# Optimization experiments

Hardware: AMD Instinct MI355X
Metric: run time of the kernel (lower is better)

Reference implementation:

```python
import jax, jax.numpy as jnp
import numpy as np

DECAY = 0.99


def setup_inputs() -> dict:
    key = jax.random.key(0)
    k1, k2, k3 = jax.random.split(key, 3)
    B, D, H, W = 16, 128, 32, 32
    K = 8192
    z_e = jax.random.normal(k1, (B, D, H, W), dtype=jnp.float32)
    codebook = jax.random.normal(k2, (K, D), dtype=jnp.float32)
    ema_count = jnp.ones((K,), dtype=jnp.float32)
    ema_weight = codebook  # buffer initialized as codebook.clone()
    return {"z_e": z_e, "codebook": codebook, "ema_count": ema_count, "ema_weight": ema_weight}


def reference(z_e, codebook, ema_count, ema_weight):
    B, D, H, W = z_e.shape
    K = codebook.shape[0]
    # (B,D,H,W) -> (N,D)
    z_flat = z_e.transpose(0, 2, 3, 1).reshape(-1, D)
    # squared L2 distances: ||z||^2 - 2 z.C^T + ||C||^2  -> (N,K)
    dist = (
        jnp.sum(z_flat * z_flat, axis=1, keepdims=True)
        - 2.0 * (z_flat @ codebook.T)
        + jnp.sum(codebook * codebook, axis=1)[None, :]
    )
    indices = jnp.argmin(dist, axis=1)  # (N,)
    z_q = codebook[indices].reshape(B, H, W, D).transpose(0, 3, 1, 2)
    # EMA codebook update (training path, no grad)
    counts = jax.ops.segment_sum(jnp.ones_like(indices, dtype=jnp.float32), indices, num_segments=K)
    dw = jax.ops.segment_sum(z_flat, indices, num_segments=K)  # (K,D)
    new_count = ema_count * DECAY + (1.0 - DECAY) * counts
    new_weight = ema_weight * DECAY + (1.0 - DECAY) * dw
    new_codebook = new_weight / jnp.maximum(new_count, 1.0)[:, None]
    # straight-through estimator
    z_q_st = z_e + jax.lax.stop_gradient(z_q - z_e)
    return (z_q_st, indices.reshape(B, H, W), new_codebook, new_count, new_weight)
```

## Files before the change

### kernel.cpp

```cpp
#include <hip/hip_runtime.h>

#define D 128
#define HW 1024
#define NROWS 16384
#define K 8192

#define OUT0 0
#define OUT1 2097152
#define OUT2 2113536
#define OUT3 3162112
#define OUT4 3170304

typedef __attribute__((ext_vector_type(8))) _Float16 half8;
typedef __attribute__((ext_vector_type(16))) float f32x16;
typedef unsigned short u16;
typedef unsigned long long u64;

__device__ __forceinline__ void gld16(const u16* gsrc, u16* ldst) {
    __builtin_amdgcn_global_load_lds(
        (const __attribute__((address_space(1))) unsigned int*)gsrc,
        (__attribute__((address_space(3))) unsigned int*)ldst,
        16, 0, 0);
}

__global__ __launch_bounds__(256) void k_cnorm(const float* __restrict__ cb,
                                               float* __restrict__ cnorm) {
    int lane = threadIdx.x & 63;
    int k = blockIdx.x * 4 + (threadIdx.x >> 6);
    float2 v = *(const float2*)(cb + (size_t)k * D + lane * 2);
    float s = v.x * v.x + v.y * v.y;
#pragma unroll
    for (int off = 32; off > 0; off >>= 1) s += __shfl_down(s, off);
    if (lane == 0) cnorm[k] = s;
}

__global__ __launch_bounds__(256) void k_prep_cb(const float* __restrict__ cb,
                                                 u16* __restrict__ Bh, u16* __restrict__ Bl) {
    int gid = blockIdx.x * 256 + threadIdx.x;
    int k  = gid & (K - 1);
    int kk = gid >> 13;
    const float* src = cb + (size_t)k * D + kk * 8;
    half8 h, l;
#pragma unroll
    for (int j = 0; j < 8; ++j) {
        float v = src[j];
        _Float16 hv = (_Float16)v;
        _Float16 lv = (_Float16)(v - (float)hv);
        h[j] = hv;
        l[j] = lv;
    }
    size_t off = ((((size_t)(k >> 8) * 8 + (kk >> 1)) * 2 + (kk & 1)) * 256 + (k & 255)) * 8;
    *(half8*)(Bh + off) = h;
    *(half8*)(Bl + off) = l;
}

__global__ __launch_bounds__(256) void k_prep_z(const float* __restrict__ z_e,
                                                u16* __restrict__ Ah, u16* __restrict__ Al) {
    int gid = blockIdx.x * 256 + threadIdx.x;
    int n  = gid & (NROWS - 1);
    int kk = gid >> 14;
    int b = n >> 10, hw = n & 1023;
    const float* src = z_e + ((size_t)b * D + kk * 8) * HW + hw;
    half8 h, l;
#pragma unroll
    for (int j = 0; j < 8; ++j) {
        float v = src[(size_t)j * HW];
        _Float16 hv = (_Float16)v;
        _Float16 lv = (_Float16)(v - (float)hv);
        h[j] = hv;
        l[j] = lv;
    }
    int rg = n >> 7, band = (n >> 5) & 3, row = n & 31;
    size_t off = (((((size_t)rg * 4 + band) * 8 + (kk >> 1)) * 2 + (kk & 1)) * 32 + row) * 8;
    *(half8*)(Ah + off) = h;
    *(half8*)(Al + off) = l;
}

__global__ __launch_bounds__(256, 1) void k_argmin_mfma(
        const u16* __restrict__ Ahg, const u16* __restrict__ Alg,
        const u16* __restrict__ Bhg, const u16* __restrict__ Blg,
        const float* __restrict__ cnorm, u64* __restrict__ packed) {
    __shared__ u16 lds[65536];
    u16* AhL = lds;
    u16* AlL = lds + 16384;
    u16* BL  = lds + 32768;

    const int tid = threadIdx.x;
    const int ln  = tid & 63;
    const int l31 = ln & 31;
    const int lh  = ln >> 5;
    const int wy  = (tid >> 6) & 1;
    const int wx  = tid >> 7;

    const int rg = blockIdx.x >> 2;
    const int k0 = (blockIdx.x & 3) * 2048;

    {
        const u16* s0 = Ahg + (size_t)rg * 16384;
        const u16* s1 = Alg + (size_t)rg * 16384;
#pragma unroll
        for (int r = 0; r < 8; ++r) {
            gld16(s0 + (r * 256 + tid) * 8, AhL + (r * 256 + tid) * 8);
            gld16(s1 + (r * 256 + tid) * 8, AlL + (r * 256 + tid) * 8);
        }
    }
    asm volatile("s_waitcnt vmcnt(0)" ::: "memory");
    __syncthreads();

    float minv[2][16];
    int   mini[2][16];
#pragma unroll
    for (int rt = 0; rt < 2; ++rt)
#pragma unroll
        for (int r = 0; r < 16; ++r) { minv[rt][r] = INFINITY; mini[rt][r] = 0; }

#pragma unroll 1
    for (int cg = 0; cg < 8; ++cg) {
        const int colbase = k0 + cg * 256;
        const size_t gB = (size_t)((k0 >> 8) + cg) * 32768;
        f32x16 acc[2][4] = {};

#pragma unroll
        for (int r = 0; r < 16; ++r)
            gld16(Blg + gB + (r * 256 + tid) * 8, BL + (r * 256 + tid) * 8);
        asm volatile("s_waitcnt vmcnt(0)" ::: "memory");
        __syncthreads();
#pragma unroll
        for (int ks = 0; ks < 8; ++ks) {
            half8 b[4], a[2];
#pragma unroll
            for (int c = 0; c < 4; ++c)
                b[c] = *(const half8*)(BL + (((ks * 2 + lh) * 256) + wx * 128 + c * 32 + l31) * 8);
#pragma unroll
            for (int rt = 0; rt < 2; ++rt)
                a[rt] = *(const half8*)(AhL + ((((wy * 2 + rt) * 8 + ks) * 2 + lh) * 32 + l31) * 8);
#pragma unroll
            for (int rt = 0; rt < 2; ++rt)
#pragma unroll
                for (int c = 0; c < 4; ++c)
                    acc[rt][c] = __builtin_amdgcn_mfma_f32_32x32x16_f16(a[rt], b[c], acc[rt][c], 0, 0, 0);
        }
        __syncthreads();

#pragma unroll
        for (int r = 0; r < 16; ++r)
            gld16(Bhg + gB + (r * 256 + tid) * 8, BL + (r * 256 + tid) * 8);

        float cn[4];
#pragma unroll
        for (int c = 0; c < 4; ++c) cn[c] = cnorm[colbase + wx * 128 + c * 32 + l31];

        asm volatile("s_waitcnt vmcnt(0)" ::: "memory");
        __syncthreads();
#pragma unroll
        for (int ks = 0; ks < 8; ++ks) {
            half8 b[4], a[2], al[2];
#pragma unroll
            for (int c = 0; c < 4; ++c)
                b[c] = *(const half8*)(BL + (((ks * 2 + lh) * 256) + wx * 128 + c * 32 + l31) * 8);
#pragma unroll
            for (int rt = 0; rt < 2; ++rt) {
                a[rt]  = *(const half8*)(AhL + ((((wy * 2 + rt) * 8 + ks) * 2 + lh) * 32 + l31) * 8);
                al[rt] = *(const half8*)(AlL + ((((wy * 2 + rt) * 8 + ks) * 2 + lh) * 32 + l31) * 8);
            }
#pragma unroll
            for (int rt = 0; rt < 2; ++rt)
#pragma unroll
                for (int c = 0; c < 4; ++c)
                    acc[rt][c] = __builtin_amdgcn_mfma_f32_32x32x16_f16(a[rt], b[c], acc[rt][c], 0, 0, 0);
#pragma unroll
            for (int rt = 0; rt < 2; ++rt)
#pragma unroll
                for (int c = 0; c < 4; ++c)
                    acc[rt][c] = __builtin_amdgcn_mfma_f32_32x32x16_f16(al[rt], b[c], acc[rt][c], 0, 0, 0);
        }

#pragma unroll
        for (int rt = 0; rt < 2; ++rt)
#pragma unroll
            for (int c = 0; c < 4; ++c) {
                const int colv = colbase + wx * 128 + c * 32 + l31;
#pragma unroll
                for (int r = 0; r < 16; ++r) {
                    float dist = fmaf(-2.0f, acc[rt][c][r], cn[c]);
                    if (dist < minv[rt][r]) { minv[rt][r] = dist; mini[rt][r] = colv; }
                }
            }
        __syncthreads();
    }

#pragma unroll
    for (int rt = 0; rt < 2; ++rt)
#pragma unroll
        for (int r = 0; r < 16; ++r) {
            float v = minv[rt][r];
            int ix = mini[rt][r];
#pragma unroll
            for (int off = 1; off < 32; off <<= 1) {
                float v2 = __shfl_xor(v, off);
                int i2 = __shfl_xor(ix, off);
                if (v2 < v || (v2 == v && i2 < ix)) { v = v2; ix = i2; }
            }
            if (l31 == 0) {
                int row = rg * 128 + wy * 64 + rt * 32 + 4 * lh + (r & 3) + 8 * (r >> 2);
                unsigned int u = __float_as_uint(v);
                u = (u & 0x80000000u) ? ~u : (u | 0x80000000u);
                u64 pk = ((u64)u << 13) | (u64)(unsigned)ix;
                atomicMin(&packed[row], pk);
            }
        }
}

__global__ __launch_bounds__(256) void k_epilogue(const float* __restrict__ z_e,
                                                  const float* __restrict__ cb,
                                                  const u64* __restrict__ packed,
                                                  float* __restrict__ out0,
                                                  float* __restrict__ out1,
                                                  float* __restrict__ counts,
                                                  float* __restrict__ dw) {
    __shared__ int idxS[64];
    const int tid = threadIdx.x;
    const int n0 = blockIdx.x * 64;
    const int bb = n0 >> 10, p0 = n0 & 1023;

    if (tid < 64) {
        int ix = (int)(packed[n0 + tid] & 0x1FFFull);
        idxS[tid] = ix;
        out1[n0 + tid] = (float)ix;
        atomicAdd(&counts[ix], 1.0f);
    }
    __syncthreads();

    const float* zb = z_e + (size_t)bb * (D * HW) + p0;
    float* ob = out0 + (size_t)bb * (D * HW) + p0;

    for (int i = tid; i < 64 * D; i += 256) {
        int d = i >> 6, r = i & 63;
        float z = zb[(size_t)d * HW + r];
        float c = cb[(size_t)idxS[r] * D + d];
        ob[(size_t)d * HW + r] = z + (c - z);
    }
    for (int i = tid; i < 64 * D; i += 256) {
        int r = i >> 7, d = i & 127;
        atomicAdd(&dw[(size_t)idxS[r] * D + d], zb[(size_t)d * HW + r]);
    }
}

__global__ __launch_bounds__(256) void k_final(const float* __restrict__ ema_count,
                                               const float* __restrict__ ema_weight,
                                               float* __restrict__ out2,
                                               float* __restrict__ out3,
                                               float* __restrict__ out4) {
    int gid = blockIdx.x * 256 + threadIdx.x;
    int k = gid >> 7, d = gid & 127;
    float cnt_raw = out3[k];
    float dw_raw = out4[gid];
    __syncthreads();
    float nc = 0.99f * ema_count[k] + 0.01f * cnt_raw;
    float nw = 0.99f * ema_weight[gid] + 0.01f * dw_raw;
    out4[gid] = nw;
    out2[gid] = nw / fmaxf(nc, 1.0f);
    if (d == 0) out3[k] = nc;
}

extern "C" void kernel_launch(void* const* d_in, const int* in_sizes, int n_in,
                              void* d_out, int out_size, void* d_ws, size_t ws_size,
                              hipStream_t stream) {
    const float* z_e        = (const float*)d_in[0];
    const float* cb         = (const float*)d_in[1];
    const float* ema_count  = (const float*)d_in[2];
    const float* ema_weight = (const float*)d_in[3];
    float* out = (float*)d_out;

    float* cnorm = (float*)d_ws;
    u64* packed = (u64*)((char*)d_ws + K * 4);

    u16* Ahg = (u16*)(out + OUT0);
    u16* Alg = Ahg + (size_t)NROWS * D;
    u16* Bhg = (u16*)(out + OUT2);
    u16* Blg = Bhg + (size_t)K * D;

    hipMemsetAsync(packed, 0xFF, NROWS * 8, stream);
    hipMemsetAsync(out + OUT3, 0, (size_t)(K + K * D) * 4, stream);

    k_cnorm      <<<K / 4,            256, 0, stream>>>(cb, cnorm);
    k_prep_cb    <<<K * 16 / 256,     256, 0, stream>>>(cb, Bhg, Blg);
    k_prep_z     <<<NROWS * 16 / 256, 256, 0, stream>>>(z_e, Ahg, Alg);
    k_argmin_mfma<<<512,              256, 0, stream>>>(Ahg, Alg, Bhg, Blg, cnorm, packed);
    k_epilogue   <<<NROWS / 64,       256, 0, stream>>>(z_e, cb, packed,
                                                        out + OUT0, out + OUT1,
                                                        out + OUT3, out + OUT4);
    k_final      <<<(K * D) / 256,    256, 0, stream>>>(ema_count, ema_weight,
                                                        out + OUT2, out + OUT3, out + OUT4);
}
```

Measured before the change: 242.5 us.

## Double-buffer codebook tiles, keep A fragments in registers, fuse norm into prep

The argmin GEMM kernel now uses 512 threads with 8 waves, each holding its 32 rows of A (hi and lo fp16 parts) in registers instead of LDS. Codebook hi/lo tiles of 128 columns are interleaved in one buffer and double-buffered in LDS with async global-to-LDS loads, so the next tile's fetch overlaps the current MFMA work. The codebook norm computation is fused into the codebook prep kernel, which removes one launch. Register pressure and occupancy change (launch bounds 512,2), and per-wave tiles are smaller, which may reduce reuse of B fragments.

```diff
diff --git a/kernel.cpp b/kernel.cpp
--- a/kernel.cpp
+++ b/kernel.cpp
@@ -4,6 +4,7 @@
 #define HW 1024
 #define NROWS 16384
 #define K 8192
+#define NU 16
 
 #define OUT0 0
 #define OUT1 2097152
@@ -23,35 +24,31 @@
         16, 0, 0);
 }
 
-__global__ __launch_bounds__(256) void k_cnorm(const float* __restrict__ cb,
-                                               float* __restrict__ cnorm) {
-    int lane = threadIdx.x & 63;
-    int k = blockIdx.x * 4 + (threadIdx.x >> 6);
-    float2 v = *(const float2*)(cb + (size_t)k * D + lane * 2);
-    float s = v.x * v.x + v.y * v.y;
-#pragma unroll
-    for (int off = 32; off > 0; off >>= 1) s += __shfl_down(s, off);
-    if (lane == 0) cnorm[k] = s;
-}
-
 __global__ __launch_bounds__(256) void k_prep_cb(const float* __restrict__ cb,
-                                                 u16* __restrict__ Bh, u16* __restrict__ Bl) {
-    int gid = blockIdx.x * 256 + threadIdx.x;
-    int k  = gid & (K - 1);
-    int kk = gid >> 13;
+                                                 u16* __restrict__ Bg,
+                                                 float* __restrict__ cnorm) {
+    int tid = threadIdx.x;
+    int kk = tid & 15;
+    int k = blockIdx.x * 16 + (tid >> 4);
     const float* src = cb + (size_t)k * D + kk * 8;
     half8 h, l;
+    float s = 0.f;
 #pragma unroll
     for (int j = 0; j < 8; ++j) {
         float v = src[j];
+        s += v * v;
         _Float16 hv = (_Float16)v;
         _Float16 lv = (_Float16)(v - (float)hv);
         h[j] = hv;
         l[j] = lv;
     }
-    size_t off = ((((size_t)(k >> 8) * 8 + (kk >> 1)) * 2 + (kk & 1)) * 256 + (k & 255)) * 8;
-    *(half8*)(Bh + off) = h;
-    *(half8*)(Bl + off) = l;
+    int g = k >> 7, col = k & 127;
+    size_t offH = (size_t)g * 32768 + ((size_t)kk * 128 + col) * 8;
+    *(half8*)((_Float16*)Bg + offH) = h;
+    *(half8*)((_Float16*)Bg + offH + 16384) = l;
+#pragma unroll
+    for (int off = 8; off > 0; off >>= 1) s += __shfl_down(s, off);
+    if (kk == 0) cnorm[k] = s;
 }
 
 __global__ __launch_bounds__(256) void k_prep_z(const float* __restrict__ z_e,
@@ -76,139 +73,116 @@
     *(half8*)(Al + off) = l;
 }
 
-__global__ __launch_bounds__(256, 1) void k_argmin_mfma(
+__global__ __launch_bounds__(512, 2) void k_argmin_mfma(
         const u16* __restrict__ Ahg, const u16* __restrict__ Alg,
-        const u16* __restrict__ Bhg, const u16* __restrict__ Blg,
+        const u16* __restrict__ Bg,
         const float* __restrict__ cnorm, u64* __restrict__ packed) {
-    __shared__ u16 lds[65536];
-    u16* AhL = lds;
-    u16* AlL = lds + 16384;
-    u16* BL  = lds + 32768;
+    __shared__ u16 lds[2][32768];
 
     const int tid = threadIdx.x;
     const int ln  = tid & 63;
     const int l31 = ln & 31;
     const int lh  = ln >> 5;
-    const int wy  = (tid >> 6) & 1;
-    const int wx  = tid >> 7;
+    const int wv  = tid >> 6;
+    const int wy  = wv & 3;
+    const int wx  = wv >> 2;
 
     const int rg = blockIdx.x >> 2;
     const int k0 = (blockIdx.x & 3) * 2048;
+    const int g0 = k0 >> 7;
+
+    half8 Ah[8], Al[8];
+#pragma unroll
+    for (int ks = 0; ks < 8; ++ks) {
+        size_t off = ((((size_t)(rg * 4 + wy) * 8 + ks) * 2 + lh) * 32 + l31) * 8;
+        Ah[ks] = *(const half8*)((const _Float16*)Ahg + off);
+        Al[ks] = *(const half8*)((const _Float16*)Alg + off);
+    }
 
     {
-        const u16* s0 = Ahg + (size_t)rg * 16384;
-        const u16* s1 = Alg + (size_t)rg * 16384;
-#pragma unroll
-        for (int r = 0; r < 8; ++r) {
-            gld16(s0 + (r * 256 + tid) * 8, AhL + (r * 256 + tid) * 8);
-            gld16(s1 + (r * 256 + tid) * 8, AlL + (r * 256 + tid) * 8);
-        }
-    }
-    asm volatile("s_waitcnt vmcnt(0)" ::: "memory");
-    __syncthreads();
-
-    float minv[2][16];
-    int   mini[2][16];
-#pragma unroll
-    for (int rt = 0; rt < 2; ++rt)
-#pragma unroll
-        for (int r = 0; r < 16; ++r) { minv[rt][r] = INFINITY; mini[rt][r] = 0; }
+        const u16* src = Bg + (size_t)g0 * 32768;
+#pragma unroll
+        for (int r = 0; r < 8; ++r)
+            gld16(src + ((size_t)r * 512 + tid) * 8, lds[0] + (r * 512 + tid) * 8);
+    }
+
+    float minv[16];
+    int   mini[16];
+#pragma unroll
+    for (int r = 0; r < 16; ++r) { minv[r] = INFINITY; mini[r] = 0; }
 
 #pragma unroll 1
-    for (int cg = 0; cg < 8; ++cg) {
-        const int colbase = k0 + cg * 256;
-        const size_t gB = (size_t)((k0 >> 8) + cg) * 32768;
-        f32x16 acc[2][4] = {};
-
-#pragma unroll
-        for (int r = 0; r < 16; ++r)
-            gld16(Blg + gB + (r * 256 + tid) * 8, BL + (r * 256 + tid) * 8);
-        asm volatile("s_waitcnt vmcnt(0)" ::: "memory");
-        __syncthreads();
+    for (int u = 0; u < NU; ++u) {
+        const u16* buf = lds[u & 1];
+        const int colbase = k0 + u * 128;
+        const int c0 = colbase + wx * 64 + l31;
+
+        float cn0 = cnorm[c0];
+        float cn1 = cnorm[c0 + 32];
+
+        if (u + 1 < NU) {
+            const u16* src = Bg + (size_t)(g0 + u + 1) * 32768;
+            u16* dst = lds[(u + 1) & 1];
+#pragma unroll
+            for (int r = 0; r < 8; ++r)
+                gld16(src + ((size_t)r * 512 + tid) * 8, dst + (r * 512 + tid) * 8);
+            asm volatile("s_waitcnt vmcnt(8)" ::: "memory");
+        } else {
+            asm volatile("s_waitcnt vmcnt(0)" ::: "memory");
+        }
+        asm volatile("s_barrier" ::: "memory");
+
+        f32x16 acc0 = {}, acc1 = {};
+        const u16* bh = buf;
+        const u16* bl = buf + 16384;
+
 #pragma unroll
         for (int ks = 0; ks < 8; ++ks) {
-            half8 b[4], a[2];
-#pragma unroll
-            for (int c = 0; c < 4; ++c)
-                b[c] = *(const half8*)(BL + (((ks * 2 + lh) * 256) + wx * 128 + c * 32 + l31) * 8);
-#pragma unroll
-            for (int rt = 0; rt < 2; ++rt)
-                a[rt] = *(const half8*)(AhL + ((((wy * 2 + rt) * 8 + ks) * 2 + lh) * 32 + l31) * 8);
-#pragma unroll
-            for (int rt = 0; rt < 2; ++rt)
-#pragma unroll
-                for (int c = 0; c < 4; ++c)
-                    acc[rt][c] = __builtin_amdgcn_mfma_f32_32x32x16_f16(a[rt], b[c], acc[rt][c], 0, 0, 0);
-        }
-        __syncthreads();
-
-#pragma unroll
-        for (int r = 0; r < 16; ++r)
-            gld16(Bhg + gB + (r * 256 + tid) * 8, BL + (r * 256 + tid) * 8);
-
-        float cn[4];
-#pragma unroll
-        for (int c = 0; c < 4; ++c) cn[c] = cnorm[colbase + wx * 128 + c * 32 + l31];
-
-        asm volatile("s_waitcnt vmcnt(0)" ::: "memory");
-        __syncthreads();
+            const int bo = ((ks * 2 + lh) * 128 + wx * 64 + l31) * 8;
+            half8 b0 = *(const half8*)((const _Float16*)bl + bo);
+            half8 b1 = *(const half8*)((const _Float16*)bl + bo + 256);
+            acc0 = __builtin_amdgcn_mfma_f32_32x32x16_f16(Ah[ks], b0, acc0, 0, 0, 0);
+            acc1 = __builtin_amdgcn_mfma_f32_32x32x16_f16(Ah[ks], b1, acc1, 0, 0, 0);
+        }
 #pragma unroll
         for (int ks = 0; ks < 8; ++ks) {
-            half8 b[4], a[2], al[2];
-#pragma unroll
-            for (int c = 0; c < 4; ++c)
-                b[c] = *(const half8*)(BL + (((ks * 2 + lh) * 256) + wx * 128 + c * 32 + l31) * 8);
-#pragma unroll
-            for (int rt = 0; rt < 2; ++rt) {
-                a[rt]  = *(const half8*)(AhL + ((((wy * 2 + rt) * 8 + ks) * 2 + lh) * 32 + l31) * 8);
-                al[rt] = *(const half8*)(AlL + ((((wy * 2 + rt) * 8 + ks) * 2 + lh) * 32 + l31) * 8);
-            }
-#pragma unroll
-            for (int rt = 0; rt < 2; ++rt)
-#pragma unroll
-                for (int c = 0; c < 4; ++c)
-                    acc[rt][c] = __builtin_amdgcn_mfma_f32_32x32x16_f16(a[rt], b[c], acc[rt][c], 0, 0, 0);
-#pragma unroll
-            for (int rt = 0; rt < 2; ++rt)
-#pragma unroll
-                for (int c = 0; c < 4; ++c)
-                    acc[rt][c] = __builtin_amdgcn_mfma_f32_32x32x16_f16(al[rt], b[c], acc[rt][c], 0, 0, 0);
-        }
-
-#pragma unroll
-        for (int rt = 0; rt < 2; ++rt)
-#pragma unroll
-            for (int c = 0; c < 4; ++c) {
-                const int colv = colbase + wx * 128 + c * 32 + l31;
-#pragma unroll
-                for (int r = 0; r < 16; ++r) {
-                    float dist = fmaf(-2.0f, acc[rt][c][r], cn[c]);
-                    if (dist < minv[rt][r]) { minv[rt][r] = dist; mini[rt][r] = colv; }
-                }
-            }
-        __syncthreads();
-    }
-
-#pragma unroll
-    for (int rt = 0; rt < 2; ++rt)
+            const int bo = ((ks * 2 + lh) * 128 + wx * 64 + l31) * 8;
+            half8 b0 = *(const half8*)((const _Float16*)bh + bo);
+            half8 b1 = *(const half8*)((const _Float16*)bh + bo + 256);
+            acc0 = __builtin_amdgcn_mfma_f32_32x32x16_f16(Ah[ks], b0, acc0, 0, 0, 0);
+            acc1 = __builtin_amdgcn_mfma_f32_32x32x16_f16(Ah[ks], b1, acc1, 0, 0, 0);
+            acc0 = __builtin_amdgcn_mfma_f32_32x32x16_f16(Al[ks], b0, acc0, 0, 0, 0);
+            acc1 = __builtin_amdgcn_mfma_f32_32x32x16_f16(Al[ks], b1, acc1, 0, 0, 0);
+        }
+
 #pragma unroll
         for (int r = 0; r < 16; ++r) {
-            float v = minv[rt][r];
-            int ix = mini[rt][r];
-#pragma unroll
-            for (int off = 1; off < 32; off <<= 1) {
-                float v2 = __shfl_xor(v, off);
-                int i2 = __shfl_xor(ix, off);
-                if (v2 < v || (v2 == v && i2 < ix)) { v = v2; ix = i2; }
-            }
-            if (l31 == 0) {
-                int row = rg * 128 + wy * 64 + rt * 32 + 4 * lh + (r & 3) + 8 * (r >> 2);
-                unsigned int u = __float_as_uint(v);
-                u = (u & 0x80000000u) ? ~u : (u | 0x80000000u);
-                u64 pk = ((u64)u << 13) | (u64)(unsigned)ix;
-                atomicMin(&packed[row], pk);
-            }
-        }
+            float d0 = fmaf(-2.0f, acc0[r], cn0);
+            float d1 = fmaf(-2.0f, acc1[r], cn1);
+            if (d0 < minv[r]) { minv[r] = d0; mini[r] = c0; }
+            if (d1 < minv[r]) { minv[r] = d1; mini[r] = c0 + 32; }
+        }
+        asm volatile("s_barrier" ::: "memory");
+    }
+
+#pragma unroll
+    for (int r = 0; r < 16; ++r) {
+        float v = minv[r];
+        int ix = mini[r];
+#pragma unroll
+        for (int off = 1; off < 32; off <<= 1) {
+            float v2 = __shfl_xor(v, off);
+            int i2 = __shfl_xor(ix, off);
+            if (v2 < v || (v2 == v && i2 < ix)) { v = v2; ix = i2; }
+        }
+        if (l31 == 0) {
+            int row = rg * 128 + wy * 32 + 4 * lh + (r & 3) + 8 * (r >> 2);
+            unsigned int uenc = __float_as_uint(v);
+            uenc = (uenc & 0x80000000u) ? ~uenc : (uenc | 0x80000000u);
+            u64 pk = ((u64)uenc << 13) | (u64)(unsigned)ix;
+            atomicMin(&packed[row], pk);
+        }
+    }
 }
 
 __global__ __launch_bounds__(256) void k_epilogue(const float* __restrict__ z_e,
@@ -277,16 +251,14 @@
 
     u16* Ahg = (u16*)(out + OUT0);
     u16* Alg = Ahg + (size_t)NROWS * D;
-    u16* Bhg = (u16*)(out + OUT2);
-    u16* Blg = Bhg + (size_t)K * D;
+    u16* Bg  = (u16*)(out + OUT2);
 
     hipMemsetAsync(packed, 0xFF, NROWS * 8, stream);
     hipMemsetAsync(out + OUT3, 0, (size_t)(K + K * D) * 4, stream);
 
-    k_cnorm      <<<K / 4,            256, 0, stream>>>(cb, cnorm);
-    k_prep_cb    <<<K * 16 / 256,     256, 0, stream>>>(cb, Bhg, Blg);
+    k_prep_cb    <<<K / 16,           256, 0, stream>>>(cb, Bg, cnorm);
     k_prep_z     <<<NROWS * 16 / 256, 256, 0, stream>>>(z_e, Ahg, Alg);
-    k_argmin_mfma<<<512,              256, 0, stream>>>(Ahg, Alg, Bhg, Blg, cnorm, packed);
+    k_argmin_mfma<<<512,              512, 0, stream>>>(Ahg, Alg, Bg, cnorm, packed);
     k_epilogue   <<<NROWS / 64,       256, 0, stream>>>(z_e, cb, packed,
                                                         out + OUT0, out + OUT1,
                                                         out + OUT3, out + OUT4);
```

Measured after the change: 220.8 us. 1.1x faster.
